# Optimization experiments

Measured on AMD Instinct MI355X. Metric: run time of the kernel, lower is better.

Reference implementation:

```python
import jax, jax.numpy as jnp
import numpy as np

B, T, NF, T2V, GH, NH, GRUH = 128, 256, 17, 16, 32, 4, 128


def _t2v(t, w0, b0, W, Bp):
    # t: [...] -> [..., T2V] = [linear term, sin periodic terms]
    lin = t[..., None] * w0 + b0
    per = jnp.sin(t[..., None] * W + Bp)
    return jnp.concatenate([lin, per], axis=-1)


def _gat(h, adj, W, a_src, a_dst, residual):
    # h: [N, F, Din], W: [Din, H, O], a_*: [H, O]; batched multi-head GAT over N graphs
    p = jnp.einsum('nfd,dho->nfho', h, W)
    es = jnp.einsum('nfho,ho->nhf', p, a_src)
    ed = jnp.einsum('nfho,ho->nhf', p, a_dst)
    e = jax.nn.leaky_relu(es[:, :, :, None] + ed[:, :, None, :], 0.2)  # [N,H,F,F]
    e = jnp.where(adj[None, None] > 0, e, jnp.float32(-1e9))
    a = jax.nn.softmax(e, axis=-1)
    out = jnp.einsum('nhij,njho->niho', a, p).reshape(h.shape[0], h.shape[1], -1)
    if residual:
        out = out + h
    return jax.nn.elu(out)


def _gru_dir(x, wih, whh, bih, bhh, reverse):
    # PyTorch GRU gate order [r, z, n]; x: [B,T,D] -> (outputs [B,T,H], h_final [B,H])
    gx = jnp.einsum('btd,gd->btg', x, wih) + bih
    if reverse:
        gx = gx[:, ::-1]
    H = whh.shape[1]

    def step(h, gxt):
        gh = h @ whh.T + bhh
        r = jax.nn.sigmoid(gxt[:, :H] + gh[:, :H])
        z = jax.nn.sigmoid(gxt[:, H:2 * H] + gh[:, H:2 * H])
        n = jnp.tanh(gxt[:, 2 * H:] + r * gh[:, 2 * H:])
        h2 = (1.0 - z) * n + z * h
        return h2, h2

    h0 = jnp.zeros((x.shape[0], H), x.dtype)
    hT, ys = jax.lax.scan(step, h0, jnp.swapaxes(gx, 0, 1))
    ys = jnp.swapaxes(ys, 0, 1)
    if reverse:
        ys = ys[:, ::-1]
    return ys, hT


def setup_inputs() -> dict:
    key = jax.random.key(0)
    ks = iter(jax.random.split(key, 64))

    def nrm(shape, fan):
        return jax.random.normal(next(ks), shape, jnp.float32) / np.float32(np.sqrt(fan))

    X = jax.random.normal(next(ks), (B, T, NF), jnp.float32)
    mask = (jax.random.uniform(next(ks), (B, T, NF)) > 0.3).astype(jnp.float32)
    delta = jax.random.uniform(next(ks), (B, T, NF), jnp.float32) * 10.0
    times = jnp.broadcast_to(jnp.arange(T, dtype=jnp.float32)[None], (B, T)) + jax.random.uniform(next(ks), (B, T), jnp.float32)
    adj = jnp.ones((NF, NF), jnp.float32) - jnp.eye(NF, dtype=jnp.float32)

    D0 = 2 + 2 * T2V  # node_in_dim = 34
    GO = GH * NH      # gat_out_dim = 128
    inp = dict(X=X, mask=mask, delta=delta, times=times, adj=adj,
               aw0=nrm((1,), 1), ab0=nrm((1,), 1), aW=nrm((T2V - 1,), 1), aB=nrm((T2V - 1,), 1),
               dw0=nrm((1,), 1), db0=nrm((1,), 1), dW=nrm((T2V - 1,), 1), dB=nrm((T2V - 1,), 1),
               gW0=nrm((D0, NH, GH), D0), gas0=nrm((NH, GH), GH), gad0=nrm((NH, GH), GH),
               gW1=nrm((GO, NH, GH), GO), gas1=nrm((NH, GH), GH), gad1=nrm((NH, GH), GH))
    for name, ind in [('g0f', GO), ('g0b', GO), ('g1f', 2 * GRUH), ('g1b', 2 * GRUH)]:
        inp[name + '_wih'] = nrm((3 * GRUH, ind), ind)
        inp[name + '_whh'] = nrm((3 * GRUH, GRUH), GRUH)
        inp[name + '_bih'] = jnp.zeros((3 * GRUH,), jnp.float32)
        inp[name + '_bhh'] = jnp.zeros((3 * GRUH,), jnp.float32)
    pd = 2 * GRUH
    inp.update(mh_w1=nrm((64, pd), pd), mh_b1=jnp.zeros((64,), jnp.float32),
               mh_w2=nrm((1, 64), 64), mh_b2=jnp.zeros((1,), jnp.float32),
               ch_w1=nrm((64, pd), pd), ch_b1=jnp.zeros((64,), jnp.float32),
               ch_w2=nrm((1, 64), 64), ch_b2=jnp.zeros((1,), jnp.float32))
    return inp


def reference(X, mask, delta, times, adj, aw0, ab0, aW, aB, dw0, db0, dW, dB,
              gW0, gas0, gad0, gW1, gas1, gad1,
              g0f_wih, g0f_whh, g0f_bih, g0f_bhh, g0b_wih, g0b_whh, g0b_bih, g0b_bhh,
              g1f_wih, g1f_whh, g1f_bih, g1f_bhh, g1b_wih, g1b_whh, g1b_bih, g1b_bhh,
              mh_w1, mh_b1, mh_w2, mh_b2, ch_w1, ch_b1, ch_w2, ch_b2):
    Bx, Tx, F = X.shape
    # node features: [x, mask, time2vec(t), time2vec(delta)] -> [B,T,F,34]
    t_emb = _t2v(times, aw0, ab0, aW, aB)
    t_emb = jnp.broadcast_to(t_emb[:, :, None, :], (Bx, Tx, F, T2V))
    d_emb = _t2v(delta, dw0, db0, dW, dB)
    nf = jnp.concatenate([X[..., None], mask[..., None], t_emb, d_emb], axis=-1)
    # batched GAT over all B*T graphs at once (replaces the Python bt-loop)
    h = nf.reshape(Bx * Tx, F, nf.shape[-1])
    h = _gat(h, adj, gW0, gas0, gad0, False)
    h = _gat(h, adj, gW1, gas1, gad1, True)
    z = h.mean(axis=1).reshape(Bx, Tx, NH * GH)
    # bidirectional 2-layer GRU
    yf, _ = _gru_dir(z, g0f_wih, g0f_whh, g0f_bih, g0f_bhh, False)
    yb, _ = _gru_dir(z, g0b_wih, g0b_whh, g0b_bih, g0b_bhh, True)
    y = jnp.concatenate([yf, yb], axis=-1)
    yf1, hf1 = _gru_dir(y, g1f_wih, g1f_whh, g1f_bih, g1f_bhh, False)
    yb1, hb1 = _gru_dir(y, g1b_wih, g1b_whh, g1b_bih, g1b_bhh, True)
    gru_out = jnp.concatenate([yf1, yb1], axis=-1)
    patient_emb = jnp.concatenate([hf1, hb1], axis=-1)
    m = jax.nn.relu(patient_emb @ mh_w1.T + mh_b1) @ mh_w2.T + mh_b2
    risk = jax.nn.relu(patient_emb @ ch_w1.T + ch_b1) @ ch_w2.T + ch_b2
    return (m, jax.nn.sigmoid(m), risk, patient_emb, gru_out)
```

## Files before the change

### kernel.cpp

```cpp
#include <hip/hip_runtime.h>
#include <hip/hip_bf16.h>
#include <math.h>

#define NFE 17
#define T2V 16
#define D0C 34
#define BB 128
#define TT 256
#define HH 128
#define ASTR 136
#define KSTR 40
#define ESTR 40
#define EHSTR 680

typedef __hip_bfloat16 bf16;
__device__ __forceinline__ float b2f(bf16 x) { return __bfloat162float(x); }

typedef __attribute__((ext_vector_type(8))) __bf16 bfrag;
typedef __attribute__((ext_vector_type(4))) float  ffrag;
typedef __attribute__((ext_vector_type(4))) __bf16 bf4;

__device__ __forceinline__ float elu_fast(float v)  { return v > 0.f ? v : __expf(v) - 1.f; }
__device__ __forceinline__ float sigm_fast(float x) { return __fdividef(1.f, 1.f + __expf(-x)); }
__device__ __forceinline__ float tanh_fast(float x) {
  return __fdividef(2.f, 1.f + __expf(-2.f*x)) - 1.f;
}

__device__ __bf16 g_W0h[8192],  g_W0l[8192];
__device__ __bf16 g_W1h[16384], g_W1l[16384];

__global__ __launch_bounds__(256) void prep_w(const float* __restrict__ W0,
                                              const float* __restrict__ W1) {
  const int tid = blockIdx.x*256 + threadIdx.x;
  if (tid < 16384) {
    const int j = tid & 7, lane = (tid >> 3) & 63, ks = (tid >> 9) & 3, nt = tid >> 11;
    const int n = nt*16 + (lane & 15), k = ks*32 + (lane >> 4)*8 + j;
    const float v = W1[k*128 + n];
    const __bf16 hi = (__bf16)v;
    g_W1h[tid] = hi;
    g_W1l[tid] = (__bf16)(v - (float)hi);
  }
  if (tid < 8192) {
    const int j = tid & 7, lane = (tid >> 3) & 63, ks = (tid >> 9) & 1, nt = tid >> 10;
    const int n = nt*16 + (lane & 15), k = ks*32 + (lane >> 4)*8 + j;
    const float v = (k < D0C) ? W0[k*128 + n] : 0.f;
    const __bf16 hi = (__bf16)v;
    g_W0h[tid] = hi;
    g_W0l[tid] = (__bf16)(v - (float)hi);
  }
}

template<int KSTEPS>
__device__ __forceinline__ void gat_proj_mfma(const __bf16* s_ah, const __bf16* s_al,
                                              const __bf16* __restrict__ Wth,
                                              const __bf16* __restrict__ Wtl,
                                              __bf16* s_pth, __bf16* s_ptl,
                                              int tid)
{
  const int lane = tid & 63, wv = tid >> 6;
  const int mn = lane & 15, q = lane >> 4;
  ffrag acc[2][2] = {};
  #pragma unroll
  for (int ks = 0; ks < KSTEPS; ++ks) {
    const bfrag ah0 = *(const bfrag*)&s_ah[(     mn)*ASTR + ks*32 + q*8];
    const bfrag al0 = *(const bfrag*)&s_al[(     mn)*ASTR + ks*32 + q*8];
    const bfrag ah1 = *(const bfrag*)&s_ah[(16 + mn)*ASTR + ks*32 + q*8];
    const bfrag al1 = *(const bfrag*)&s_al[(16 + mn)*ASTR + ks*32 + q*8];
    #pragma unroll
    for (int nt = 0; nt < 2; ++nt) {
      const int fi = (((wv*2 + nt)*KSTEPS + ks)*64 + lane)*8;
      const bfrag bh = *(const bfrag*)&Wth[fi];
      const bfrag bl = *(const bfrag*)&Wtl[fi];
      acc[0][nt] = __builtin_amdgcn_mfma_f32_16x16x32_bf16(al0, bh, acc[0][nt], 0,0,0);
      acc[0][nt] = __builtin_amdgcn_mfma_f32_16x16x32_bf16(ah0, bl, acc[0][nt], 0,0,0);
      acc[0][nt] = __builtin_amdgcn_mfma_f32_16x16x32_bf16(ah0, bh, acc[0][nt], 0,0,0);
      acc[1][nt] = __builtin_amdgcn_mfma_f32_16x16x32_bf16(al1, bh, acc[1][nt], 0,0,0);
      acc[1][nt] = __builtin_amdgcn_mfma_f32_16x16x32_bf16(ah1, bl, acc[1][nt], 0,0,0);
      acc[1][nt] = __builtin_amdgcn_mfma_f32_16x16x32_bf16(ah1, bh, acc[1][nt], 0,0,0);
    }
  }
  const int n0 = wv*32;
  #pragma unroll
  for (int nt = 0; nt < 2; ++nt) {
    const int col = n0 + nt*16 + mn;
    __bf16 hbuf[4], lbuf[4];
    #pragma unroll
    for (int i = 0; i < 4; ++i) {
      const float v = acc[0][nt][i];
      const __bf16 hi = (__bf16)v;
      hbuf[i] = hi;
      lbuf[i] = (__bf16)(v - (float)hi);
    }
    *(bf4*)&s_pth[col*KSTR + q*4] = *(bf4*)hbuf;
    *(bf4*)&s_ptl[col*KSTR + q*4] = *(bf4*)lbuf;
    if (q == 0) {
      const float v = acc[1][nt][0];
      const __bf16 hi = (__bf16)v;
      s_pth[col*KSTR + 16] = hi;
      s_ptl[col*KSTR + 16] = (__bf16)(v - (float)hi);
    }
  }
}

__device__ __forceinline__ void gat_scoresm(const __bf16* s_pth, const __bf16* s_ptl,
                                            const float* __restrict__ asrc,
                                            const float* __restrict__ adst,
                                            const float* s_adj,
                                            __bf16* s_Eh, __bf16* s_El, int tid) {
  const int lane = tid & 63, h = tid >> 6;
  const int f = lane & 31;
  float sc = 0.f;
  if (f < NFE) {
    const float* av = (lane < 32) ? asrc : adst;
    const int base = h*32*KSTR + f;
    #pragma unroll
    for (int o = 0; o < 32; ++o) {
      const float p = (float)s_pth[base + o*KSTR] + (float)s_ptl[base + o*KSTR];
      sc = fmaf(p, av[h*32 + o], sc);
    }
  }
  float ed[NFE];
  #pragma unroll
  for (int j = 0; j < NFE; ++j) ed[j] = __shfl(sc, 32 + j);
  if (lane < NFE) {
    const int i = lane;
    const float esv = sc;
    float row[NFE]; float mx = -1e30f;
    #pragma unroll
    for (int j = 0; j < NFE; ++j) {
      float v = -1.0e9f;
      if (s_adj[i*NFE + j] > 0.f) {
        const float e = esv + ed[j];
        v = (e > 0.f) ? e : 0.2f*e;
      }
      row[j] = v; mx = fmaxf(mx, v);
    }
    float sum = 0.f;
    #pragma unroll
    for (int j = 0; j < NFE; ++j) { row[j] = __expf(row[j] - mx); sum += row[j]; }
    const float inv = __fdividef(1.f, sum);
    __bf16 hrow[32], lrow[32];
    #pragma unroll
    for (int j = 0; j < 32; ++j) {
      const float v = (j < NFE) ? row[j]*inv : 0.f;
      const __bf16 hi = (__bf16)v;
      hrow[j] = hi;
      lrow[j] = (__bf16)(v - (float)hi);
    }
    #pragma unroll
    for (int w = 0; w < 4; ++w) {
      *(bfrag*)&s_Eh[h*EHSTR + i*ESTR + w*8] = *(bfrag*)&hrow[w*8];
      *(bfrag*)&s_El[h*EHSTR + i*ESTR + w*8] = *(bfrag*)&lrow[w*8];
    }
  }
}

__device__ __forceinline__ void gat_out_core(const __bf16* s_Eh, const __bf16* s_El,
                                             const __bf16* s_pth, const __bf16* s_ptl,
                                             int wv, int mn, int q, ffrag acc[2][2]) {
  const bfrag eh0 = *(const bfrag*)&s_Eh[wv*EHSTR + mn*ESTR + q*8];
  const bfrag el0 = *(const bfrag*)&s_El[wv*EHSTR + mn*ESTR + q*8];
  const bfrag eh1 = *(const bfrag*)&s_Eh[wv*EHSTR + (16+mn)*ESTR + q*8];
  const bfrag el1 = *(const bfrag*)&s_El[wv*EHSTR + (16+mn)*ESTR + q*8];
  #pragma unroll
  for (int nt = 0; nt < 2; ++nt) {
    const int nrow = wv*32 + nt*16 + mn;
    const bfrag ph = *(const bfrag*)&s_pth[nrow*KSTR + q*8];
    const bfrag pl = *(const bfrag*)&s_ptl[nrow*KSTR + q*8];
    acc[0][nt] = __builtin_amdgcn_mfma_f32_16x16x32_bf16(el0, ph, acc[0][nt], 0,0,0);
    acc[0][nt] = __builtin_amdgcn_mfma_f32_16x16x32_bf16(eh0, pl, acc[0][nt], 0,0,0);
    acc[0][nt] = __builtin_amdgcn_mfma_f32_16x16x32_bf16(eh0, ph, acc[0][nt], 0,0,0);
    acc[1][nt] = __builtin_amdgcn_mfma_f32_16x16x32_bf16(el1, ph, acc[1][nt], 0,0,0);
    acc[1][nt] = __builtin_amdgcn_mfma_f32_16x16x32_bf16(eh1, pl, acc[1][nt], 0,0,0);
    acc[1][nt] = __builtin_amdgcn_mfma_f32_16x16x32_bf16(eh1, ph, acc[1][nt], 0,0,0);
  }
}

__device__ __forceinline__ void gat_out0(const __bf16* s_Eh, const __bf16* s_El,
                                         const __bf16* s_pth, const __bf16* s_ptl,
                                         __bf16* s_ah, __bf16* s_al, int tid) {
  const int lane = tid & 63, wv = tid >> 6;
  const int mn = lane & 15, q = lane >> 4;
  ffrag acc[2][2] = {};
  gat_out_core(s_Eh, s_El, s_pth, s_ptl, wv, mn, q, acc);
  #pragma unroll
  for (int nt = 0; nt < 2; ++nt) {
    const int c = wv*32 + nt*16 + mn;
    #pragma unroll
    for (int i = 0; i < 4; ++i) {
      const float v = elu_fast(acc[0][nt][i]);
      const __bf16 hi = (__bf16)v;
      s_ah[(q*4+i)*ASTR + c] = hi;
      s_al[(q*4+i)*ASTR + c] = (__bf16)(v - (float)hi);
    }
    if (q == 0) {
      const float v = elu_fast(acc[1][nt][0]);
      const __bf16 hi = (__bf16)v;
      s_ah[16*ASTR + c] = hi;
      s_al[16*ASTR + c] = (__bf16)(v - (float)hi);
    }
  }
}

__device__ __forceinline__ void gat_out1(const __bf16* s_Eh, const __bf16* s_El,
                                         const __bf16* s_pth, const __bf16* s_ptl,
                                         const __bf16* s_ah, const __bf16* s_al,
                                         float* __restrict__ zrow, int tid) {
  const int lane = tid & 63, wv = tid >> 6;
  const int mn = lane & 15, q = lane >> 4;
  ffrag acc[2][2] = {};
  gat_out_core(s_Eh, s_El, s_pth, s_ptl, wv, mn, q, acc);
  #pragma unroll
  for (int nt = 0; nt < 2; ++nt) {
    const int c = wv*32 + nt*16 + mn;
    float sum = 0.f;
    #pragma unroll
    for (int i = 0; i < 4; ++i) {
      const int r = q*4 + i;
      const float res = (float)s_ah[r*ASTR + c] + (float)s_al[r*ASTR + c];
      sum += elu_fast(acc[0][nt][i] + res);
    }
    sum += __shfl_xor(sum, 16);
    sum += __shfl_xor(sum, 32);
    if (q == 0) {
      const float res = (float)s_ah[16*ASTR + c] + (float)s_al[16*ASTR + c];
      sum += elu_fast(acc[1][nt][0] + res);
      zrow[c] = sum * (1.0f/17.0f);
    }
  }
}

__global__ __launch_bounds__(256) void gat_fused(
    const float* __restrict__ X,  const float* __restrict__ Mk,
    const float* __restrict__ Dl, const float* __restrict__ Tm,
    const float* __restrict__ Adj,
    const float* __restrict__ aw0, const float* __restrict__ ab0,
    const float* __restrict__ aW,  const float* __restrict__ aB,
    const float* __restrict__ dw0, const float* __restrict__ db0,
    const float* __restrict__ dW,  const float* __restrict__ dB,
    const float* __restrict__ as0, const float* __restrict__ ad0,
    const float* __restrict__ as1, const float* __restrict__ ad1,
    float* __restrict__ zslot)
{
  __shared__ __align__(16) unsigned char smem[41828];
  __bf16* s_ah  = (__bf16*)(smem);
  __bf16* s_al  = (__bf16*)(smem + 4624);
  __bf16* s_Eh  = (__bf16*)(smem + 9248);
  __bf16* s_El  = (__bf16*)(smem + 14688);
  __bf16* s_pth = (__bf16*)(smem + 20128);
  __bf16* s_ptl = (__bf16*)(smem + 30368);
  float*  s_t   = (float*)(smem + 40608);
  float*  s_adj = (float*)(smem + 40672);
  const int n = blockIdx.x;
  const int tid = threadIdx.x;

  {
    const float4 z4 = {0.f, 0.f, 0.f, 0.f};
    float4* zp = (float4*)(smem + 20128);
    for (int i = tid; i < 1280; i += 256) zp[i] = z4;
  }
  const float tv = Tm[n];
  if (tid < T2V) {
    s_t[tid] = (tid == 0) ? fmaf(tv, aw0[0], ab0[0])
                          : __sinf(fmaf(tv, aW[tid-1], aB[tid-1]));
  }
  for (int idx = tid; idx < NFE*NFE; idx += 256) s_adj[idx] = Adj[idx];
  __syncthreads();
  for (int idx = tid; idx < NFE*64; idx += 256) {
    const int f = idx >> 6, c = idx & 63;
    float v = 0.f;
    if (c == 0)            v = X [(size_t)n*NFE + f];
    else if (c == 1)       v = Mk[(size_t)n*NFE + f];
    else if (c < 2 + T2V)  v = s_t[c-2];
    else if (c < D0C) {
      const float dd = Dl[(size_t)n*NFE + f];
      const int j = c - (2 + T2V);
      v = (j == 0) ? fmaf(dd, dw0[0], db0[0])
                   : __sinf(fmaf(dd, dW[j-1], dB[j-1]));
    }
    const __bf16 hi = (__bf16)v;
    s_ah[f*ASTR + c] = hi;
    s_al[f*ASTR + c] = (__bf16)(v - (float)hi);
  }
  __syncthreads();
  gat_proj_mfma<2>(s_ah, s_al, g_W0h, g_W0l, s_pth, s_ptl, tid);     __syncthreads();
  gat_scoresm(s_pth, s_ptl, as0, ad0, s_adj, s_Eh, s_El, tid);       __syncthreads();
  gat_out0(s_Eh, s_El, s_pth, s_ptl, s_ah, s_al, tid);               __syncthreads();
  gat_proj_mfma<4>(s_ah, s_al, g_W1h, g_W1l, s_pth, s_ptl, tid);     __syncthreads();
  gat_scoresm(s_pth, s_ptl, as1, ad1, s_adj, s_Eh, s_El, tid);       __syncthreads();
  gat_out1(s_Eh, s_El, s_pth, s_ptl, s_ah, s_al,
           zslot + (size_t)n*256 + 128, tid);
}

__global__ __launch_bounds__(256) void gemm_xw_mfma(
    const float* __restrict__ A, int lda,
    const float* __restrict__ Wf, const float* __restrict__ biasf,
    bf16* __restrict__ Cf,
    const float* __restrict__ Wb, const float* __restrict__ biasb,
    bf16* __restrict__ Cb, int K)
{
  const float* W    = blockIdx.z ? Wb : Wf;
  const float* bias = blockIdx.z ? biasb : biasf;
  bf16*        C    = blockIdx.z ? Cb : Cf;
  __shared__ __bf16 Ah[64][40];
  __shared__ __bf16 Al[64][40];
  __shared__ __bf16 Wh[64][40];
  __shared__ __bf16 Wl[64][40];
  const int tid = threadIdx.x;
  const int bm0 = blockIdx.x * 64;
  const int bn0 = blockIdx.y * 64;
  const int lane = tid & 63, wv = tid >> 6;
  const int mn = lane & 15, q = lane >> 4;
  const int sr = tid >> 2, sk = (tid & 3) * 8;
  ffrag acc[4] = {};
  for (int kk = 0; kk < K; kk += 32) {
    {
      float av[8];
      *(float4*)&av[0] = *(const float4*)&A[(size_t)(bm0 + sr)*lda + kk + sk];
      *(float4*)&av[4] = *(const float4*)&A[(size_t)(bm0 + sr)*lda + kk + sk + 4];
      __bf16 th[8], tl[8];
      #pragma unroll
      for (int i = 0; i < 8; ++i) {
        const __bf16 hi = (__bf16)av[i];
        th[i] = hi;
        tl[i] = (__bf16)(av[i] - (float)hi);
      }
      *(bfrag*)&Ah[sr][sk] = *(bfrag*)th;
      *(bfrag*)&Al[sr][sk] = *(bfrag*)tl;
      float wv8[8];
      *(float4*)&wv8[0] = *(const float4*)&W[(size_t)(bn0 + sr)*K + kk + sk];
      *(float4*)&wv8[4] = *(const float4*)&W[(size_t)(bn0 + sr)*K + kk + sk + 4];
      __bf16 wh8[8], wl8[8];
      #pragma unroll
      for (int i = 0; i < 8; ++i) {
        const __bf16 hi = (__bf16)wv8[i];
        wh8[i] = hi;
        wl8[i] = (__bf16)(wv8[i] - (float)hi);
      }
      *(bfrag*)&Wh[sr][sk] = *(bfrag*)wh8;
      *(bfrag*)&Wl[sr][sk] = *(bfrag*)wl8;
    }
    __syncthreads();
    const bfrag afh = *(const bfrag*)&Ah[16*wv + mn][q*8];
    const bfrag afl = *(const bfrag*)&Al[16*wv + mn][q*8];
    #pragma unroll
    for (int t = 0; t < 4; ++t) {
      const bfrag bwh = *(const bfrag*)&Wh[16*t + mn][q*8];
      const bfrag bwl = *(const bfrag*)&Wl[16*t + mn][q*8];
      acc[t] = __builtin_amdgcn_mfma_f32_16x16x32_bf16(afl, bwh, acc[t], 0, 0, 0);
      acc[t] = __builtin_amdgcn_mfma_f32_16x16x32_bf16(afh, bwl, acc[t], 0, 0, 0);
      acc[t] = __builtin_amdgcn_mfma_f32_16x16x32_bf16(afh, bwh, acc[t], 0, 0, 0);
    }
    __syncthreads();
  }
  #pragma unroll
  for (int t = 0; t < 4; ++t) {
    const int col = bn0 + 16*t + mn;
    const float bv = bias[col];
    #pragma unroll
    for (int i = 0; i < 4; ++i) {
      const int row = bm0 + 16*wv + q*4 + i;
      C[(size_t)row*384 + col] = __float2bfloat16(acc[t][i] + bv);
    }
  }
}

__global__ __launch_bounds__(768, 1) void gru_rec(
    const bf16* __restrict__ gxf,
    const bf16* __restrict__ gxb,
    const float* __restrict__ whh_f, const float* __restrict__ whh_b,
    const float* __restrict__ bhh_f, const float* __restrict__ bhh_b,
    float* __restrict__ ys,
    float* __restrict__ hfin)
{
  const int blk = blockIdx.x;
  const int dir = blk >> 7;
  const int b   = blk & 127;
  const int g   = threadIdx.x;
  const int p   = threadIdx.y;
  const float* whh = dir ? whh_b : whh_f;
  const float* bhh = dir ? bhh_b : bhh_f;
  const bf16* gx   = (dir ? gxb : gxf) + (size_t)b*TT*384;
  __shared__ __align__(16) float s_h[HH];
  __shared__ float s_gh  [3*HH];
  __shared__ float s_part[3*HH];
  __shared__ float s_gx  [3*HH];
  float4 w[HH/8];
  #pragma unroll
  for (int d4 = 0; d4 < HH/8; ++d4)
    w[d4] = *(const float4*)&whh[(size_t)g*HH + p*64 + 4*d4];
  const float bh = p ? 0.f : bhh[g];
  float hreg = 0.f;
  if (p == 0 && g < HH) s_h[g] = 0.f;
  __syncthreads();
  for (int s = 0; s < TT; ++s) {
    const int t = dir ? (TT-1-s) : s;
    float gxv = 0.f;
    if (p == 0) gxv = b2f(gx[(size_t)t*384 + g]);
    float acc = bh;
    const float4* h4 = (const float4*)&s_h[p*64];
    #pragma unroll
    for (int d4 = 0; d4 < HH/8; ++d4) {
      const float4 hv = h4[d4];
      acc = fmaf(hv.x, w[d4].x, acc);
      acc = fmaf(hv.y, w[d4].y, acc);
      acc = fmaf(hv.z, w[d4].z, acc);
      acc = fmaf(hv.w, w[d4].w, acc);
    }
    if (p == 0) { s_gh[g] = acc; s_gx[g] = gxv; }
    else        { s_part[g] = acc; }
    __syncthreads();
    if (p == 0 && g < HH) {
      const float r  = sigm_fast(s_gx[g]      + s_gh[g]      + s_part[g]);
      const float zg = sigm_fast(s_gx[HH+g]   + s_gh[HH+g]   + s_part[HH+g]);
      const float nn = tanh_fast(s_gx[2*HH+g] + r*(s_gh[2*HH+g] + s_part[2*HH+g]));
      hreg = (1.f - zg)*nn + zg*hreg;
      s_h[g] = hreg;
      ys[((size_t)b*TT + t)*256 + dir*HH + g] = hreg;
    }
    __syncthreads();
  }
  if (p == 0 && g < HH && hfin) hfin[(size_t)b*256 + dir*HH + g] = hreg;
}

__global__ __launch_bounds__(64) void heads_k(
    const float* __restrict__ pemb,
    const float* __restrict__ mw1, const float* __restrict__ mb1,
    const float* __restrict__ mw2, const float* __restrict__ mb2,
    const float* __restrict__ cw1, const float* __restrict__ cb1,
    const float* __restrict__ cw2, const float* __restrict__ cb2,
    float* __restrict__ out)
{
  const int b = blockIdx.x, tid = threadIdx.x;
  __shared__ float sh[64];
  const float* pe = pemb + (size_t)b*256;
  float acc = mb1[tid];
  for (int d = 0; d < 256; ++d) acc = fmaf(pe[d], mw1[(size_t)tid*256 + d], acc);
  sh[tid] = fmaxf(acc, 0.f) * mw2[tid];
  __syncthreads();
  if (tid == 0) {
    float s = mb2[0];
    for (int i = 0; i < 64; ++i) s += sh[i];
    out[b]       = s;
    out[128 + b] = 1.f/(1.f + expf(-s));
  }
  __syncthreads();
  acc = cb1[tid];
  for (int d = 0; d < 256; ++d) acc = fmaf(pe[d], cw1[(size_t)tid*256 + d], acc);
  sh[tid] = fmaxf(acc, 0.f) * cw2[tid];
  __syncthreads();
  if (tid == 0) {
    float s = cb2[0];
    for (int i = 0; i < 64; ++i) s += sh[i];
    out[256 + b] = s;
  }
}

extern "C" void kernel_launch(void* const* d_in, const int* in_sizes, int n_in,
                              void* d_out, int out_size, void* d_ws, size_t ws_size,
                              hipStream_t stream) {
  const float* X    = (const float*)d_in[0];
  const float* Mk   = (const float*)d_in[1];
  const float* Dl   = (const float*)d_in[2];
  const float* Tm   = (const float*)d_in[3];
  const float* Adj  = (const float*)d_in[4];
  const float* aw0  = (const float*)d_in[5];
  const float* ab0  = (const float*)d_in[6];
  const float* aWt  = (const float*)d_in[7];
  const float* aBt  = (const float*)d_in[8];
  const float* dw0  = (const float*)d_in[9];
  const float* db0  = (const float*)d_in[10];
  const float* dWt  = (const float*)d_in[11];
  const float* dBt  = (const float*)d_in[12];
  const float* gW0  = (const float*)d_in[13];
  const float* gas0 = (const float*)d_in[14];
  const float* gad0 = (const float*)d_in[15];
  const float* gW1  = (const float*)d_in[16];
  const float* gas1 = (const float*)d_in[17];
  const float* gad1 = (const float*)d_in[18];
  const float* g0f_wih = (const float*)d_in[19];
  const float* g0f_whh = (const float*)d_in[20];
  const float* g0f_bih = (const float*)d_in[21];
  const float* g0f_bhh = (const float*)d_in[22];
  const float* g0b_wih = (const float*)d_in[23];
  const float* g0b_whh = (const float*)d_in[24];
  const float* g0b_bih = (const float*)d_in[25];
  const float* g0b_bhh = (const float*)d_in[26];
  const float* g1f_wih = (const float*)d_in[27];
  const float* g1f_whh = (const float*)d_in[28];
  const float* g1f_bih = (const float*)d_in[29];
  const float* g1f_bhh = (const float*)d_in[30];
  const float* g1b_wih = (const float*)d_in[31];
  const float* g1b_whh = (const float*)d_in[32];
  const float* g1b_bih = (const float*)d_in[33];
  const float* g1b_bhh = (const float*)d_in[34];
  const float* mh_w1 = (const float*)d_in[35];
  const float* mh_b1 = (const float*)d_in[36];
  const float* mh_w2 = (const float*)d_in[37];
  const float* mh_b2 = (const float*)d_in[38];
  const float* ch_w1 = (const float*)d_in[39];
  const float* ch_b1 = (const float*)d_in[40];
  const float* ch_w2 = (const float*)d_in[41];
  const float* ch_b2 = (const float*)d_in[42];

  bf16* gxA = (bf16*)d_ws;
  bf16* gxB = gxA + 12582912;

  float* out  = (float*)d_out;
  float* pemb = out + 384;
  float* slot = out + 384 + 32768;

  prep_w<<<64, 256, 0, stream>>>(gW0, gW1);

  gat_fused<<<dim3(BB*TT), dim3(256), 0, stream>>>(
      X, Mk, Dl, Tm, Adj, aw0, ab0, aWt, aBt, dw0, db0, dWt, dBt,
      gas0, gad0, gas1, gad1, slot);

  dim3 ggrid(32768/64, 384/64, 2);
  gemm_xw_mfma<<<ggrid, 256, 0, stream>>>(slot + 128, 256,
      g0f_wih, g0f_bih, gxA, g0b_wih, g0b_bih, gxB, 128);
  gru_rec<<<256, dim3(384, 2), 0, stream>>>(gxA, gxB, g0f_whh, g0b_whh,
                                            g0f_bhh, g0b_bhh, slot, nullptr);
  gemm_xw_mfma<<<ggrid, 256, 0, stream>>>(slot, 256,
      g1f_wih, g1f_bih, gxA, g1b_wih, g1b_bih, gxB, 256);
  gru_rec<<<256, dim3(384, 2), 0, stream>>>(gxA, gxB, g1f_whh, g1b_whh,
                                            g1f_bhh, g1b_bhh, slot, pemb);

  heads_k<<<128, 64, 0, stream>>>(pemb, mh_w1, mh_b1, mh_w2, mh_b2,
                                  ch_w1, ch_b1, ch_w2, ch_b2, out);
}
```

Before: 1.224 ms.

## Fold GAT attention vectors into projection weights to compute scores via MFMA

Precomputes W·a_src and W·a_dst per head in the weight-prep kernel and appends them as an extra 16-column tile to the split-bf16 weight layout. Wave 0 then produces the source and destination attention scores directly from the projection MFMA, so the per-node scalar dot-product loop over shared-memory projections is removed. Softmax reads the scores from small shared arrays. This adds extra MFMA work on one wave, which may imbalance the waves, and changes rounding because scores are computed from hi/lo bf16 products of folded weights.

```diff
diff --git a/kernel.cpp b/kernel.cpp
--- a/kernel.cpp
+++ b/kernel.cpp
@@ -26,24 +26,46 @@
   return __fdividef(2.f, 1.f + __expf(-2.f*x)) - 1.f;
 }
 
-__device__ __bf16 g_W0h[8192],  g_W0l[8192];
-__device__ __bf16 g_W1h[16384], g_W1l[16384];
-
-__global__ __launch_bounds__(256) void prep_w(const float* __restrict__ W0,
-                                              const float* __restrict__ W1) {
+__device__ __bf16 g_W0h[9216],  g_W0l[9216];
+__device__ __bf16 g_W1h[18432], g_W1l[18432];
+
+__global__ __launch_bounds__(256) void prep_w(
+    const float* __restrict__ W0, const float* __restrict__ W1,
+    const float* __restrict__ as0, const float* __restrict__ ad0,
+    const float* __restrict__ as1, const float* __restrict__ ad1) {
   const int tid = blockIdx.x*256 + threadIdx.x;
-  if (tid < 16384) {
+  if (tid < 18432) {
     const int j = tid & 7, lane = (tid >> 3) & 63, ks = (tid >> 9) & 3, nt = tid >> 11;
-    const int n = nt*16 + (lane & 15), k = ks*32 + (lane >> 4)*8 + j;
-    const float v = W1[k*128 + n];
+    const int c = lane & 15, k = ks*32 + (lane >> 4)*8 + j;
+    float v = 0.f;
+    if (nt < 8) {
+      v = W1[k*128 + nt*16 + c];
+    } else if (c < 8) {
+      const int h = c & 3;
+      const float* av = (c < 4) ? as1 : ad1;
+      #pragma unroll
+      for (int o = 0; o < 32; ++o)
+        v = fmaf(W1[k*128 + h*32 + o], av[h*32 + o], v);
+    }
     const __bf16 hi = (__bf16)v;
     g_W1h[tid] = hi;
     g_W1l[tid] = (__bf16)(v - (float)hi);
   }
-  if (tid < 8192) {
+  if (tid < 9216) {
     const int j = tid & 7, lane = (tid >> 3) & 63, ks = (tid >> 9) & 1, nt = tid >> 10;
-    const int n = nt*16 + (lane & 15), k = ks*32 + (lane >> 4)*8 + j;
-    const float v = (k < D0C) ? W0[k*128 + n] : 0.f;
+    const int c = lane & 15, k = ks*32 + (lane >> 4)*8 + j;
+    float v = 0.f;
+    if (k < D0C) {
+      if (nt < 8) {
+        v = W0[k*128 + nt*16 + c];
+      } else if (c < 8) {
+        const int h = c & 3;
+        const float* av = (c < 4) ? as0 : ad0;
+        #pragma unroll
+        for (int o = 0; o < 32; ++o)
+          v = fmaf(W0[k*128 + h*32 + o], av[h*32 + o], v);
+      }
+    }
     const __bf16 hi = (__bf16)v;
     g_W0h[tid] = hi;
     g_W0l[tid] = (__bf16)(v - (float)hi);
@@ -55,11 +77,12 @@
                                               const __bf16* __restrict__ Wth,
                                               const __bf16* __restrict__ Wtl,
                                               __bf16* s_pth, __bf16* s_ptl,
-                                              int tid)
+                                              float* s_es, float* s_ed, int tid)
 {
   const int lane = tid & 63, wv = tid >> 6;
   const int mn = lane & 15, q = lane >> 4;
   ffrag acc[2][2] = {};
+  ffrag acc2[2] = {};
   #pragma unroll
   for (int ks = 0; ks < KSTEPS; ++ks) {
     const bfrag ah0 = *(const bfrag*)&s_ah[(     mn)*ASTR + ks*32 + q*8];
@@ -78,6 +101,17 @@
       acc[1][nt] = __builtin_amdgcn_mfma_f32_16x16x32_bf16(ah1, bl, acc[1][nt], 0,0,0);
       acc[1][nt] = __builtin_amdgcn_mfma_f32_16x16x32_bf16(ah1, bh, acc[1][nt], 0,0,0);
     }
+    if (wv == 0) {
+      const int fi = ((8*KSTEPS + ks)*64 + lane)*8;
+      const bfrag bh = *(const bfrag*)&Wth[fi];
+      const bfrag bl = *(const bfrag*)&Wtl[fi];
+      acc2[0] = __builtin_amdgcn_mfma_f32_16x16x32_bf16(al0, bh, acc2[0], 0,0,0);
+      acc2[0] = __builtin_amdgcn_mfma_f32_16x16x32_bf16(ah0, bl, acc2[0], 0,0,0);
+      acc2[0] = __builtin_amdgcn_mfma_f32_16x16x32_bf16(ah0, bh, acc2[0], 0,0,0);
+      acc2[1] = __builtin_amdgcn_mfma_f32_16x16x32_bf16(al1, bh, acc2[1], 0,0,0);
+      acc2[1] = __builtin_amdgcn_mfma_f32_16x16x32_bf16(ah1, bl, acc2[1], 0,0,0);
+      acc2[1] = __builtin_amdgcn_mfma_f32_16x16x32_bf16(ah1, bh, acc2[1], 0,0,0);
+    }
   }
   const int n0 = wv*32;
   #pragma unroll
@@ -100,37 +134,29 @@
       s_ptl[col*KSTR + 16] = (__bf16)(v - (float)hi);
     }
   }
-}
-
-__device__ __forceinline__ void gat_scoresm(const __bf16* s_pth, const __bf16* s_ptl,
-                                            const float* __restrict__ asrc,
-                                            const float* __restrict__ adst,
+  if (wv == 0 && mn < 8) {
+    const int h = mn & 3;
+    float* dst = (mn >= 4) ? s_ed : s_es;
+    #pragma unroll
+    for (int i = 0; i < 4; ++i)
+      dst[h*NFE + q*4 + i] = acc2[0][i];
+    if (q == 0) dst[h*NFE + 16] = acc2[1][0];
+  }
+}
+
+__device__ __forceinline__ void gat_softmax(const float* s_es, const float* s_ed,
                                             const float* s_adj,
                                             __bf16* s_Eh, __bf16* s_El, int tid) {
   const int lane = tid & 63, h = tid >> 6;
-  const int f = lane & 31;
-  float sc = 0.f;
-  if (f < NFE) {
-    const float* av = (lane < 32) ? asrc : adst;
-    const int base = h*32*KSTR + f;
-    #pragma unroll
-    for (int o = 0; o < 32; ++o) {
-      const float p = (float)s_pth[base + o*KSTR] + (float)s_ptl[base + o*KSTR];
-      sc = fmaf(p, av[h*32 + o], sc);
-    }
-  }
-  float ed[NFE];
-  #pragma unroll
-  for (int j = 0; j < NFE; ++j) ed[j] = __shfl(sc, 32 + j);
   if (lane < NFE) {
     const int i = lane;
-    const float esv = sc;
+    const float esv = s_es[h*NFE + i];
     float row[NFE]; float mx = -1e30f;
     #pragma unroll
     for (int j = 0; j < NFE; ++j) {
       float v = -1.0e9f;
       if (s_adj[i*NFE + j] > 0.f) {
-        const float e = esv + ed[j];
+        const float e = esv + s_ed[h*NFE + j];
         v = (e > 0.f) ? e : 0.2f*e;
       }
       row[j] = v; mx = fmaxf(mx, v);
@@ -238,19 +264,19 @@
     const float* __restrict__ aW,  const float* __restrict__ aB,
     const float* __restrict__ dw0, const float* __restrict__ db0,
     const float* __restrict__ dW,  const float* __restrict__ dB,
-    const float* __restrict__ as0, const float* __restrict__ ad0,
-    const float* __restrict__ as1, const float* __restrict__ ad1,
     float* __restrict__ zslot)
 {
-  __shared__ __align__(16) unsigned char smem[41828];
+  __shared__ __align__(16) unsigned char smem[42372];
   __bf16* s_ah  = (__bf16*)(smem);
   __bf16* s_al  = (__bf16*)(smem + 4624);
   __bf16* s_Eh  = (__bf16*)(smem + 9248);
   __bf16* s_El  = (__bf16*)(smem + 14688);
   __bf16* s_pth = (__bf16*)(smem + 20128);
   __bf16* s_ptl = (__bf16*)(smem + 30368);
-  float*  s_t   = (float*)(smem + 40608);
-  float*  s_adj = (float*)(smem + 40672);
+  float*  s_es  = (float*)(smem + 40608);
+  float*  s_ed  = (float*)(smem + 40880);
+  float*  s_t   = (float*)(smem + 41152);
+  float*  s_adj = (float*)(smem + 41216);
   const int n = blockIdx.x;
   const int tid = threadIdx.x;
 
@@ -283,11 +309,16 @@
     s_al[f*ASTR + c] = (__bf16)(v - (float)hi);
   }
   __syncthreads();
-  gat_proj_mfma<2>(s_ah, s_al, g_W0h, g_W0l, s_pth, s_ptl, tid);     __syncthreads();
-  gat_scoresm(s_pth, s_ptl, as0, ad0, s_adj, s_Eh, s_El, tid);       __syncthreads();
-  gat_out0(s_Eh, s_El, s_pth, s_ptl, s_ah, s_al, tid);               __syncthreads();
-  gat_proj_mfma<4>(s_ah, s_al, g_W1h, g_W1l, s_pth, s_ptl, tid);     __syncthreads();
-  gat_scoresm(s_pth, s_ptl, as1, ad1, s_adj, s_Eh, s_El, tid);       __syncthreads();
+  gat_proj_mfma<2>(s_ah, s_al, g_W0h, g_W0l, s_pth, s_ptl, s_es, s_ed, tid);
+  __syncthreads();
+  gat_softmax(s_es, s_ed, s_adj, s_Eh, s_El, tid);
+  __syncthreads();
+  gat_out0(s_Eh, s_El, s_pth, s_ptl, s_ah, s_al, tid);
+  __syncthreads();
+  gat_proj_mfma<4>(s_ah, s_al, g_W1h, g_W1l, s_pth, s_ptl, s_es, s_ed, tid);
+  __syncthreads();
+  gat_softmax(s_es, s_ed, s_adj, s_Eh, s_El, tid);
+  __syncthreads();
   gat_out1(s_Eh, s_El, s_pth, s_ptl, s_ah, s_al,
            zslot + (size_t)n*256 + 128, tid);
 }
@@ -510,11 +541,10 @@
   float* pemb = out + 384;
   float* slot = out + 384 + 32768;
 
-  prep_w<<<64, 256, 0, stream>>>(gW0, gW1);
+  prep_w<<<72, 256, 0, stream>>>(gW0, gW1, gas0, gad0, gas1, gad1);
 
   gat_fused<<<dim3(BB*TT), dim3(256), 0, stream>>>(
-      X, Mk, Dl, Tm, Adj, aw0, ab0, aWt, aBt, dw0, db0, dWt, dBt,
-      gas0, gad0, gas1, gad1, slot);
+      X, Mk, Dl, Tm, Adj, aw0, ab0, aWt, aBt, dw0, db0, dWt, dBt, slot);
 
   dim3 ggrid(32768/64, 384/64, 2);
   gemm_xw_mfma<<<ggrid, 256, 0, stream>>>(slot + 128, 256,
```

After: 1.240 ms. Within noise of the previous version (+1.3%).
